# Kernel tuning notes

Measured on AMD Instinct MI355X. Metric: run time of the kernel, lower is better.

Reference implementation:

```python
import jax, jax.numpy as jnp
import numpy as np

D_MODEL = 1024
N_HEADS = 16
D_K = D_MODEL // N_HEADS


def setup_inputs() -> dict:
    key = jax.random.key(0)
    ks = jax.random.split(key, 9)
    s = 1.0 / np.sqrt(D_MODEL)
    x = jax.random.normal(ks[0], (4, 2048, D_MODEL), dtype=jnp.float32)
    def lin(kw, kb):
        W = jax.random.uniform(kw, (D_MODEL, D_MODEL), jnp.float32, -s, s)
        b = jax.random.uniform(kb, (D_MODEL,), jnp.float32, -s, s)
        return W, b
    W_q, b_q = lin(ks[1], ks[2])
    W_k, b_k = lin(ks[3], ks[4])
    W_v, b_v = lin(ks[5], ks[6])
    W_o, b_o = lin(ks[7], ks[8])
    return {"x": x, "W_q": W_q, "b_q": b_q, "W_k": W_k, "b_k": b_k,
            "W_v": W_v, "b_v": b_v, "W_o": W_o, "b_o": b_o}


def reference(x, W_q, b_q, W_k, b_k, W_v, b_v, W_o, b_o):
    B, S, D = x.shape
    # projections: torch Linear computes x @ W.T + b
    Q = x @ W_q.T + b_q
    K = x @ W_k.T + b_k
    V = x @ W_v.T + b_v
    # split heads -> [B, H, S, d_k]
    Q = Q.reshape(B, S, N_HEADS, D_K).transpose(0, 2, 1, 3)
    K = K.reshape(B, S, N_HEADS, D_K).transpose(0, 2, 1, 3)
    V = V.reshape(B, S, N_HEADS, D_K).transpose(0, 2, 1, 3)
    scale = float(np.sqrt(D_K))
    scores = jnp.einsum('bhqd,bhkd->bhqk', Q, K) / scale
    # max-subtract + softmax == stable softmax (no mask, dropout is eval no-op)
    attn = jax.nn.softmax(scores, axis=-1)
    context = jnp.einsum('bhqk,bhkd->bhqd', attn, V)
    context = context.transpose(0, 2, 1, 3).reshape(B, S, D)
    return context @ W_o.T + b_o
```

## Files before the change

### kernel.cpp

```cpp
#include <hip/hip_runtime.h>
#include <hip/hip_bf16.h>
#include <cstdint>

#define D_MODEL 1024
#define N_HEADS 16
#define SEQ     2048
#define BATCH   4
#define M_TOT   (BATCH*SEQ)

typedef short bf16x8 __attribute__((ext_vector_type(8)));
typedef float f32x4  __attribute__((ext_vector_type(4)));
typedef __hip_bfloat16 bf16;

__device__ __forceinline__ void gld_lds16(const void* g, void* l) {
    __builtin_amdgcn_global_load_lds(
        (const __attribute__((address_space(1))) void*)(uintptr_t)g,
        (__attribute__((address_space(3))) void*)(uint32_t)(uintptr_t)l,
        16, 0, 0);
}

__global__ __launch_bounds__(256)
void cvt_all(const float* __restrict__ x,  const float* __restrict__ Wq,
             const float* __restrict__ Wk, const float* __restrict__ Wv,
             const float* __restrict__ Wo,
             bf16* __restrict__ xb, bf16* __restrict__ Wqb,
             bf16* __restrict__ Wkb, bf16* __restrict__ Wvb,
             bf16* __restrict__ Wob)
{
    const size_t CH = (size_t)1024*1024;
    int c = blockIdx.y;
    const float* src; bf16* dst;
    if (c < 8)       { src = x  + (size_t)c*CH; dst = xb  + (size_t)c*CH; }
    else if (c == 8) { src = Wq; dst = Wqb; }
    else if (c == 9) { src = Wk; dst = Wkb; }
    else if (c ==10) { src = Wv; dst = Wvb; }
    else             { src = Wo; dst = Wob; }
    int i = (blockIdx.x * 256 + threadIdx.x) * 8;
    float4 a = *(const float4*)(src + i);
    float4 b = *(const float4*)(src + i + 4);
    union { bf16 h[8]; uint4 v; } pk;
    pk.h[0] = __float2bfloat16(a.x); pk.h[1] = __float2bfloat16(a.y);
    pk.h[2] = __float2bfloat16(a.z); pk.h[3] = __float2bfloat16(a.w);
    pk.h[4] = __float2bfloat16(b.x); pk.h[5] = __float2bfloat16(b.y);
    pk.h[6] = __float2bfloat16(b.z); pk.h[7] = __float2bfloat16(b.w);
    *(uint4*)(dst + i) = pk.v;
}

template<int MODE>
__device__ __forceinline__
void gemm128_body(const bf16* __restrict__ A, const bf16* __restrict__ W,
                  const float* __restrict__ bias, void* __restrict__ Cout,
                  float scale, int m0, int n0w, int n0c, bf16* As, bf16* Bs)
{
    constexpr int K = D_MODEL, N = D_MODEL;
    const int tid  = threadIdx.x;
    const int wv   = tid >> 6;
    const int lane = tid & 63;
    const int quad = lane >> 4;
    const int l16  = lane & 15;
    const int l8   = l16 & 7;
    const int wr   = wv >> 1, wc = wv & 1;

    const int srow_off = lane >> 3;
    const int sgc      = (lane & 7) ^ srow_off;

    f32x4 acc[4][4];
    #pragma unroll
    for (int i = 0; i < 4; ++i)
        #pragma unroll
        for (int j = 0; j < 4; ++j) acc[i][j] = (f32x4){0.f,0.f,0.f,0.f};

    for (int k0 = 0; k0 < K; k0 += 64) {
        __syncthreads();
        #pragma unroll
        for (int r = 0; r < 4; ++r) {
            int row0 = wv*32 + r*8;
            gld_lds16(A + (size_t)(m0  + row0 + srow_off)*K + k0 + sgc*8,
                      As + row0*64);
            gld_lds16(W + (size_t)(n0w + row0 + srow_off)*K + k0 + sgc*8,
                      Bs + row0*64);
        }
        __syncthreads();
        #pragma unroll
        for (int ks = 0; ks < 2; ++ks) {
            bf16x8 af[4], bfb[4];
            #pragma unroll
            for (int i = 0; i < 4; ++i)
                af[i] = *(const bf16x8*)(As + (wr*64 + i*16 + l16)*64
                                         + (((ks*4 + quad) ^ l8))*8);
            #pragma unroll
            for (int j = 0; j < 4; ++j)
                bfb[j] = *(const bf16x8*)(Bs + (wc*64 + j*16 + l16)*64
                                          + (((ks*4 + quad) ^ l8))*8);
            #pragma unroll
            for (int i = 0; i < 4; ++i)
                #pragma unroll
                for (int j = 0; j < 4; ++j)
                    acc[i][j] = __builtin_amdgcn_mfma_f32_16x16x32_bf16(af[i], bfb[j], acc[i][j], 0,0,0);
        }
    }

    #pragma unroll
    for (int j = 0; j < 4; ++j) {
        int n = n0c + wc*64 + j*16 + l16;
        float bv = bias[n];
        #pragma unroll
        for (int i = 0; i < 4; ++i) {
            if constexpr (MODE == 2) {
                union { bf16 hh[4]; uint2 u; } pk;
                #pragma unroll
                for (int r = 0; r < 4; ++r)
                    pk.hh[r] = __float2bfloat16((acc[i][j][r] + bv) * scale);
                int mb = m0 + wr*64 + i*16 + quad*4;
                *(uint2*)((bf16*)Cout + (size_t)n*M_TOT + mb) = pk.u;
            } else {
                #pragma unroll
                for (int r = 0; r < 4; ++r) {
                    int m = m0 + wr*64 + i*16 + quad*4 + r;
                    float v = (acc[i][j][r] + bv) * scale;
                    if constexpr (MODE == 0)
                        ((bf16*)Cout)[(size_t)m*N + n] = __float2bfloat16(v);
                    else
                        ((float*)Cout)[(size_t)m*N + n] = v;
                }
            }
        }
    }
}

#define QSCALE (0.125f * 1.44269504089f)

__global__ __launch_bounds__(256)
void gemm_qkv(const bf16* __restrict__ xb, const bf16* __restrict__ Wcat,
              const float* __restrict__ bq, const float* __restrict__ bk,
              const float* __restrict__ bv,
              bf16* __restrict__ Qp, bf16* __restrict__ Kp, bf16* __restrict__ VT)
{
    __shared__ __attribute__((aligned(16))) bf16 As[128*64];
    __shared__ __attribute__((aligned(16))) bf16 Bs[128*64];
    const int m0 = blockIdx.x * 128, n0w = blockIdx.y * 128;
    const int sel = n0w >> 10, n0c = n0w & 1023;
    if (sel == 0)
        gemm128_body<0>(xb, Wcat, bq, Qp, QSCALE, m0, n0w, n0c, As, Bs);
    else if (sel == 1)
        gemm128_body<0>(xb, Wcat, bk, Kp, 1.0f, m0, n0w, n0c, As, Bs);
    else
        gemm128_body<2>(xb, Wcat, bv, VT, 1.0f, m0, n0w, n0c, As, Bs);
}

__global__ __launch_bounds__(256)
void gemm_out(const bf16* __restrict__ Cp, const bf16* __restrict__ Wo,
              const float* __restrict__ bo, float* __restrict__ out)
{
    __shared__ __attribute__((aligned(16))) bf16 As[128*64];
    __shared__ __attribute__((aligned(16))) bf16 Bs[128*64];
    const int n0 = blockIdx.y * 128;
    gemm128_body<1>(Cp, Wo, bo, out, 1.0f, blockIdx.x*128, n0, n0, As, Bs);
}

__global__ __launch_bounds__(256)
void flash_attn9(const bf16* __restrict__ Q, const bf16* __restrict__ Kp,
                 const bf16* __restrict__ VT, bf16* __restrict__ ctx)
{
    __shared__ __attribute__((aligned(16))) bf16 Ks[64*64];
    __shared__ __attribute__((aligned(16))) bf16 Vs[64*64];
    __shared__ __attribute__((aligned(16))) bf16 Ps[128*64];

    const int tid  = threadIdx.x;
    const int wv   = tid >> 6;
    const int lane = tid & 63;
    const int quad = lane >> 4;
    const int l16  = lane & 15;
    const int l8   = l16 & 7;

    const int b  = blockIdx.z;
    const int h  = blockIdx.y;
    const int q0 = blockIdx.x * 128;

    const bf16* kbase = Kp + (size_t)(b*SEQ)*D_MODEL + h*64;
    const bf16* vbase = VT + (size_t)(h*64)*M_TOT + (size_t)b*SEQ;

    const int srow_off = lane >> 3;
    const int sgc      = (lane & 7) ^ srow_off;

    bf16x8 aq[2][2];
    #pragma unroll
    for (int g = 0; g < 2; ++g) {
        const bf16* qp = Q + (size_t)(b*SEQ + q0 + wv*32 + g*16 + l16)*D_MODEL + h*64;
        aq[g][0] = *(const bf16x8*)(qp + quad*8);
        aq[g][1] = *(const bf16x8*)(qp + 32 + quad*8);
    }

    float l_lane[2] = {0.f, 0.f};
    f32x4 o[2][4];
    #pragma unroll
    for (int g = 0; g < 2; ++g)
        #pragma unroll
        for (int j = 0; j < 4; ++j) o[g][j] = (f32x4){0.f,0.f,0.f,0.f};

    for (int kt = 0; kt < SEQ/64; ++kt) {
        __syncthreads();
        #pragma unroll
        for (int t = 0; t < 2; ++t) {
            int row0 = wv*16 + t*8;
            gld_lds16(kbase + (size_t)(kt*64 + row0 + srow_off)*D_MODEL + sgc*8,
                      &Ks[row0*64]);
            gld_lds16(vbase + (size_t)(row0 + srow_off)*M_TOT + kt*64 + sgc*8,
                      &Vs[row0*64]);
        }
        __syncthreads();

        #pragma unroll
        for (int ktile = 0; ktile < 4; ++ktile) {
            bf16x8 ak[2];
            #pragma unroll
            for (int ks = 0; ks < 2; ++ks)
                ak[ks] = *(const bf16x8*)(&Ks[(ktile*16 + l16)*64
                                          + ((ks*4 + quad) ^ l8)*8]);
            #pragma unroll
            for (int g = 0; g < 2; ++g) {
                f32x4 st = (f32x4){0.f,0.f,0.f,0.f};
                st = __builtin_amdgcn_mfma_f32_16x16x32_bf16(ak[0], aq[g][0], st, 0,0,0);
                st = __builtin_amdgcn_mfma_f32_16x16x32_bf16(ak[1], aq[g][1], st, 0,0,0);
                union { bf16 hh[4]; uint2 u; } pk;
                #pragma unroll
                for (int r = 0; r < 4; ++r) {
                    float p = __builtin_amdgcn_exp2f(st[r]);
                    l_lane[g] += p;
                    pk.hh[r] = __float2bfloat16(p);
                }
                *(uint2*)(&Ps[(wv*32 + g*16 + l16)*64
                              + ((ktile*2 + (quad>>1)) ^ l8)*8 + (quad&1)*4]) = pk.u;
            }
        }

        #pragma unroll
        for (int g = 0; g < 2; ++g)
            #pragma unroll
            for (int ks = 0; ks < 2; ++ks) {
                bf16x8 ap = *(const bf16x8*)(&Ps[(wv*32 + g*16 + l16)*64
                                             + ((ks*4 + quad) ^ l8)*8]);
                #pragma unroll
                for (int j = 0; j < 4; ++j) {
                    bf16x8 bv = *(const bf16x8*)(&Vs[(j*16 + l16)*64
                                                 + ((ks*4 + quad) ^ l8)*8]);
                    o[g][j] = __builtin_amdgcn_mfma_f32_16x16x32_bf16(ap, bv, o[g][j], 0,0,0);
                }
            }
    }

    #pragma unroll
    for (int g = 0; g < 2; ++g) {
        float l = l_lane[g];
        l += __shfl_xor(l, 16);
        l += __shfl_xor(l, 32);
        #pragma unroll
        for (int r = 0; r < 4; ++r) {
            float inv = 1.f / __shfl(l, quad*4 + r, 16);
            int q = q0 + wv*32 + g*16 + quad*4 + r;
            #pragma unroll
            for (int j = 0; j < 4; ++j)
                ctx[(size_t)(b*SEQ + q)*D_MODEL + h*64 + j*16 + l16] =
                    __float2bfloat16(o[g][j][r] * inv);
        }
    }
}

extern "C" void kernel_launch(void* const* d_in, const int* in_sizes, int n_in,
                              void* d_out, int out_size, void* d_ws, size_t ws_size,
                              hipStream_t stream)
{
    const float* x  = (const float*)d_in[0];
    const float* Wq = (const float*)d_in[1];
    const float* bq = (const float*)d_in[2];
    const float* Wk = (const float*)d_in[3];
    const float* bk = (const float*)d_in[4];
    const float* Wv = (const float*)d_in[5];
    const float* bv = (const float*)d_in[6];
    const float* Wo = (const float*)d_in[7];
    const float* bo = (const float*)d_in[8];

    const size_t NEL = (size_t)M_TOT * D_MODEL;
    const size_t WEL = (size_t)D_MODEL * D_MODEL;

    bf16* ws  = (bf16*)d_ws;
    bf16* xb  = ws;
    bf16* Wqb = ws + NEL;
    bf16* Wkb = Wqb + WEL;
    bf16* Wvb = Wkb + WEL;
    bf16* Wob = Wvb + WEL;
    bf16* Qp  = Wob + WEL;
    bf16* Kp  = Qp + NEL;
    bf16* VT  = Kp + NEL;
    bf16* Cp  = VT + NEL;
    float* out = (float*)d_out;

    dim3 blk(256);
    hipLaunchKernelGGL(cvt_all, dim3(512, 12), blk, 0, stream,
                       x, Wq, Wk, Wv, Wo, xb, Wqb, Wkb, Wvb, Wob);
    hipLaunchKernelGGL(gemm_qkv, dim3(M_TOT/128, 3*D_MODEL/128), blk, 0, stream,
                       xb, Wqb, bq, bk, bv, Qp, Kp, VT);
    hipLaunchKernelGGL(flash_attn9, dim3(SEQ/128, N_HEADS, BATCH), blk, 0, stream,
                       Qp, Kp, VT, Cp);
    hipLaunchKernelGGL(gemm_out, dim3(M_TOT/128, D_MODEL/128), blk, 0, stream,
                       Cp, Wob, bo, out);
}
```

Measured before the change: 293.4 us.

## Double-buffer K/V tiles and keep P in registers for PV MFMA

The attention kernel now double-buffers the K and V tiles in LDS and prefetches the next tile while computing the current one, which removes one barrier per iteration. The softmax probabilities stay in registers and feed 16x16x16 MFMAs directly, so the Ps LDS round-trip is gone. The cost is more LDS for the K/V buffers and twice as many smaller MFMA instructions for the PV product. The prefetch relies on a single barrier per iteration and on global_load_lds completing before the next barrier.

```diff
diff --git a/kernel.cpp b/kernel.cpp
--- a/kernel.cpp
+++ b/kernel.cpp
@@ -9,6 +9,7 @@
 #define M_TOT   (BATCH*SEQ)
 
 typedef short bf16x8 __attribute__((ext_vector_type(8)));
+typedef short bf16x4 __attribute__((ext_vector_type(4)));
 typedef float f32x4  __attribute__((ext_vector_type(4)));
 typedef __hip_bfloat16 bf16;
 
@@ -159,12 +160,11 @@
 }
 
 __global__ __launch_bounds__(256)
-void flash_attn9(const bf16* __restrict__ Q, const bf16* __restrict__ Kp,
-                 const bf16* __restrict__ VT, bf16* __restrict__ ctx)
-{
-    __shared__ __attribute__((aligned(16))) bf16 Ks[64*64];
-    __shared__ __attribute__((aligned(16))) bf16 Vs[64*64];
-    __shared__ __attribute__((aligned(16))) bf16 Ps[128*64];
+void flash_attn11(const bf16* __restrict__ Q, const bf16* __restrict__ Kp,
+                  const bf16* __restrict__ VT, bf16* __restrict__ ctx)
+{
+    __shared__ __attribute__((aligned(16))) bf16 Ks[2][64*64];
+    __shared__ __attribute__((aligned(16))) bf16 Vs[2][64*64];
 
     const int tid  = threadIdx.x;
     const int wv   = tid >> 6;
@@ -198,54 +198,63 @@
         #pragma unroll
         for (int j = 0; j < 4; ++j) o[g][j] = (f32x4){0.f,0.f,0.f,0.f};
 
+    #pragma unroll
+    for (int t = 0; t < 2; ++t) {
+        int row0 = wv*16 + t*8;
+        gld_lds16(kbase + (size_t)(row0 + srow_off)*D_MODEL + sgc*8,
+                  &Ks[0][row0*64]);
+        gld_lds16(vbase + (size_t)(row0 + srow_off)*M_TOT + sgc*8,
+                  &Vs[0][row0*64]);
+    }
+
     for (int kt = 0; kt < SEQ/64; ++kt) {
+        const int cur = kt & 1;
         __syncthreads();
-        #pragma unroll
-        for (int t = 0; t < 2; ++t) {
-            int row0 = wv*16 + t*8;
-            gld_lds16(kbase + (size_t)(kt*64 + row0 + srow_off)*D_MODEL + sgc*8,
-                      &Ks[row0*64]);
-            gld_lds16(vbase + (size_t)(row0 + srow_off)*M_TOT + kt*64 + sgc*8,
-                      &Vs[row0*64]);
-        }
-        __syncthreads();
-
+        if (kt + 1 < SEQ/64) {
+            #pragma unroll
+            for (int t = 0; t < 2; ++t) {
+                int row0 = wv*16 + t*8;
+                gld_lds16(kbase + (size_t)((kt+1)*64 + row0 + srow_off)*D_MODEL + sgc*8,
+                          &Ks[cur^1][row0*64]);
+                gld_lds16(vbase + (size_t)(row0 + srow_off)*M_TOT + (kt+1)*64 + sgc*8,
+                          &Vs[cur^1][row0*64]);
+            }
+        }
+
+        bf16x4 paf[2][4];
         #pragma unroll
         for (int ktile = 0; ktile < 4; ++ktile) {
             bf16x8 ak[2];
             #pragma unroll
             for (int ks = 0; ks < 2; ++ks)
-                ak[ks] = *(const bf16x8*)(&Ks[(ktile*16 + l16)*64
+                ak[ks] = *(const bf16x8*)(&Ks[cur][(ktile*16 + l16)*64
                                           + ((ks*4 + quad) ^ l8)*8]);
             #pragma unroll
             for (int g = 0; g < 2; ++g) {
                 f32x4 st = (f32x4){0.f,0.f,0.f,0.f};
                 st = __builtin_amdgcn_mfma_f32_16x16x32_bf16(ak[0], aq[g][0], st, 0,0,0);
                 st = __builtin_amdgcn_mfma_f32_16x16x32_bf16(ak[1], aq[g][1], st, 0,0,0);
-                union { bf16 hh[4]; uint2 u; } pk;
+                union { bf16 hh[4]; bf16x4 v; } pk;
                 #pragma unroll
                 for (int r = 0; r < 4; ++r) {
                     float p = __builtin_amdgcn_exp2f(st[r]);
                     l_lane[g] += p;
                     pk.hh[r] = __float2bfloat16(p);
                 }
-                *(uint2*)(&Ps[(wv*32 + g*16 + l16)*64
-                              + ((ktile*2 + (quad>>1)) ^ l8)*8 + (quad&1)*4]) = pk.u;
+                paf[g][ktile] = pk.v;
             }
         }
 
         #pragma unroll
-        for (int g = 0; g < 2; ++g)
-            #pragma unroll
-            for (int ks = 0; ks < 2; ++ks) {
-                bf16x8 ap = *(const bf16x8*)(&Ps[(wv*32 + g*16 + l16)*64
-                                             + ((ks*4 + quad) ^ l8)*8]);
-                #pragma unroll
-                for (int j = 0; j < 4; ++j) {
-                    bf16x8 bv = *(const bf16x8*)(&Vs[(j*16 + l16)*64
-                                                 + ((ks*4 + quad) ^ l8)*8]);
-                    o[g][j] = __builtin_amdgcn_mfma_f32_16x16x32_bf16(ap, bv, o[g][j], 0,0,0);
-                }
+        for (int ktile = 0; ktile < 4; ++ktile)
+            #pragma unroll
+            for (int jt = 0; jt < 4; ++jt) {
+                bf16x4 bv = *(const bf16x4*)(&Vs[cur][(jt*16 + l16)*64
+                              + ((ktile*2 + (quad>>1)) ^ l8)*8 + (quad&1)*4]);
+                #pragma unroll
+                for (int g = 0; g < 2; ++g)
+                    o[g][jt] = __builtin_amdgcn_mfma_f32_16x16x16bf16_1k(
+                                   paf[g][ktile], bv, o[g][jt], 0, 0, 0);
             }
     }
 
@@ -300,7 +309,7 @@
                        x, Wq, Wk, Wv, Wo, xb, Wqb, Wkb, Wvb, Wob);
     hipLaunchKernelGGL(gemm_qkv, dim3(M_TOT/128, 3*D_MODEL/128), blk, 0, stream,
                        xb, Wqb, bq, bk, bv, Qp, Kp, VT);
-    hipLaunchKernelGGL(flash_attn9, dim3(SEQ/128, N_HEADS, BATCH), blk, 0, stream,
+    hipLaunchKernelGGL(flash_attn11, dim3(SEQ/128, N_HEADS, BATCH), blk, 0, stream,
                        Qp, Kp, VT, Cp);
     hipLaunchKernelGGL(gemm_out, dim3(M_TOT/128, D_MODEL/128), blk, 0, stream,
                        Cp, Wob, bo, out);
```

New measurement: 287.3 us. 1.02x faster.
